# Optimization experiments

Measured on AMD Instinct MI355X. Metric: run time of the kernel, lower is better.

Reference implementation:

```python
import jax, jax.numpy as jnp
import numpy as np

D_MODEL = 1024
H = 16
HEAD_DIM = D_MODEL // H  # 64


def setup_inputs() -> dict:
    key = jax.random.key(0)
    ks = jax.random.split(key, 11)
    B, S, D = 1, 4096, D_MODEL
    scale = 1.0 / np.sqrt(D)
    inp = {
        'q': jax.random.normal(ks[0], (B, S, D), jnp.float32),
        'k': jax.random.normal(ks[1], (B, S, D), jnp.float32),
        'v': jax.random.normal(ks[2], (B, S, D), jnp.float32),
        'w_q': jax.random.normal(ks[3], (D, D), jnp.float32) * scale,
        'b_q': jnp.zeros((D,), jnp.float32),
        'w_k': jax.random.normal(ks[4], (D, D), jnp.float32) * scale,
        'b_k': jnp.zeros((D,), jnp.float32),
        'w_v': jax.random.normal(ks[5], (D, D), jnp.float32) * scale,
        'b_v': jnp.zeros((D,), jnp.float32),
        'w_o': jax.random.normal(ks[6], (D, D), jnp.float32) * scale,
        'b_o': jnp.zeros((D,), jnp.float32),
    }
    return inp


def reference(q, k, v, w_q, b_q, w_k, b_k, w_v, b_v, w_o, b_o):
    B, Sq, D = q.shape
    Sk = k.shape[1]
    # Linear projections (torch Linear: x @ W.T + b), split into heads: [B,H,S,hd]
    Q = (q @ w_q.T + b_q).reshape(B, Sq, H, HEAD_DIM).transpose(0, 2, 1, 3)
    K = (k @ w_k.T + b_k).reshape(B, Sk, H, HEAD_DIM).transpose(0, 2, 1, 3)
    V = (v @ w_v.T + b_v).reshape(B, Sk, H, HEAD_DIM).transpose(0, 2, 1, 3)
    # Naive attention: full [B,H,Sq,Sk] scores, softmax, then AV
    scores = jnp.einsum('bhqd,bhkd->bhqk', Q, K) / jnp.sqrt(jnp.float32(HEAD_DIM))
    attn = jax.nn.softmax(scores, axis=-1)
    ctx = jnp.einsum('bhqk,bhkd->bhqd', attn, V)
    concat = ctx.transpose(0, 2, 1, 3).reshape(B, Sq, D)
    return concat @ w_o.T + b_o
```

## Files before the change

### kernel.cpp

```cpp
#include <hip/hip_runtime.h>
#include <stdint.h>

#define S_LEN 4096
#define DM 1024
#define NH 16

typedef __attribute__((ext_vector_type(8))) short short8;
typedef __attribute__((ext_vector_type(4))) short short4v;
typedef __attribute__((ext_vector_type(4))) float float4v;
typedef __attribute__((ext_vector_type(4))) unsigned short ushort4v;

typedef __attribute__((address_space(1))) const void* as1cvp;
typedef __attribute__((address_space(3))) void* as3vp;

#define MFMA16(a, b, c) __builtin_amdgcn_mfma_f32_16x16x32_bf16((a), (b), (c), 0, 0, 0)
#define MFMA16K16(a, b, c) __builtin_amdgcn_mfma_f32_16x16x16bf16_1k((a), (b), (c), 0, 0, 0)
#define GLOAD_LDS16(g, l) \
  __builtin_amdgcn_global_load_lds((as1cvp)(g), (as3vp)(l), 16, 0, 0)

__device__ __forceinline__ unsigned short f2bf(float f) {
  unsigned u = __float_as_uint(f);
  u += 0x7fffu + ((u >> 16) & 1u);
  return (unsigned short)(u >> 16);
}

__device__ __forceinline__ float exp2_hw(float x) {
  float r;
  asm("v_exp_f32 %0, %1" : "=v"(r) : "v"(x));
  return r;
}

__global__ __launch_bounds__(256) void cast_all(
    const float* __restrict__ q, const float* __restrict__ k, const float* __restrict__ v,
    const float* __restrict__ wq, const float* __restrict__ wk, const float* __restrict__ wv,
    const float* __restrict__ wo, unsigned short* __restrict__ dst)
{
  const float* src; size_t off; int n;
  switch (blockIdx.y) {
    case 0: src = q;  off = 0u;        n = 4194304; break;
    case 1: src = k;  off = 4194304u;  n = 4194304; break;
    case 2: src = v;  off = 8388608u;  n = 4194304; break;
    case 3: src = wq; off = 12582912u; n = 1048576; break;
    case 4: src = wk; off = 13631488u; n = 1048576; break;
    case 5: src = wv; off = 14680064u; n = 1048576; break;
    default: src = wo; off = 15728640u; n = 1048576; break;
  }
  int nv = n >> 2;
  for (int i = blockIdx.x * blockDim.x + threadIdx.x; i < nv; i += gridDim.x * blockDim.x) {
    float4v val = ((const float4v*)src)[i];
    ushort4v o;
    o.x = f2bf(val.x); o.y = f2bf(val.y); o.z = f2bf(val.z); o.w = f2bf(val.w);
    ((ushort4v*)(dst + off))[i] = o;
  }
}

template<int MODE>
__device__ __forceinline__ void gemm128(
    const unsigned short* __restrict__ A, const unsigned short* __restrict__ Bw,
    unsigned short* Cb, float* Cf, const float* __restrict__ bias, float alpha,
    unsigned short* As, unsigned short* Bs)
{
  const int K = 1024, N = 1024;
  int bm = blockIdx.x, bn = blockIdx.y;
  int t = threadIdx.x, lane = t & 63, w = t >> 6;
  int l15 = lane & 15, l4 = lane >> 4;
  int wr = w >> 1, wc = w & 1;

  float4v acc[4][4] = {};

  for (int kt = 0; kt < K / 32; ++kt) {
#pragma unroll
    for (int i = 0; i < 2; ++i) {
      int ci = i * 256 + t;
      int r = ci >> 2, cb = ci & 3;
      GLOAD_LDS16(A + (size_t)(bm * 128 + r) * K + kt * 32 + cb * 8,
                  As + (size_t)(i * 256 + w * 64) * 8);
      GLOAD_LDS16(Bw + (size_t)(bn * 128 + r) * K + kt * 32 + cb * 8,
                  Bs + (size_t)(i * 256 + w * 64) * 8);
    }
    __syncthreads();
    short8 af[4], bfr[4];
#pragma unroll
    for (int mf = 0; mf < 4; ++mf)
      af[mf] = *(const short8*)&As[(wr * 64 + mf * 16 + l15) * 32 + l4 * 8];
#pragma unroll
    for (int nf = 0; nf < 4; ++nf)
      bfr[nf] = *(const short8*)&Bs[(wc * 64 + nf * 16 + l15) * 32 + l4 * 8];
#pragma unroll
    for (int mf = 0; mf < 4; ++mf)
#pragma unroll
      for (int nf = 0; nf < 4; ++nf)
        acc[mf][nf] = MFMA16(af[mf], bfr[nf], acc[mf][nf]);
    __syncthreads();
  }

#pragma unroll
  for (int mf = 0; mf < 4; ++mf)
#pragma unroll
    for (int nf = 0; nf < 4; ++nf) {
      int col = bn * 128 + wc * 64 + nf * 16 + l15;
      float bv = bias[col];
#pragma unroll
      for (int j = 0; j < 4; ++j) {
        int row = bm * 128 + wr * 64 + mf * 16 + l4 * 4 + j;
        float val = (acc[mf][nf][j] + bv) * alpha;
        if (MODE == 1)      Cf[(size_t)row * N + col] = val;
        else if (MODE == 2) Cb[(size_t)col * S_LEN + row] = f2bf(val);
        else                Cb[(size_t)row * N + col] = f2bf(val);
      }
    }
}

__global__ __launch_bounds__(256) void proj_qkv(
    const unsigned short* xq, const unsigned short* xk, const unsigned short* xv,
    const unsigned short* wq, const unsigned short* wk, const unsigned short* wv,
    unsigned short* Qp, unsigned short* Kp, unsigned short* Vt,
    const float* bq, const float* bk, const float* bv)
{
  __shared__ unsigned short As[128 * 32], Bs[128 * 32];
  switch (blockIdx.z) {
    case 0:  gemm128<0>(xq, wq, Qp, nullptr, bq, 0.1803368867f, As, Bs); break;
    case 1:  gemm128<0>(xk, wk, Kp, nullptr, bk, 1.0f,          As, Bs); break;
    default: gemm128<2>(xv, wv, Vt, nullptr, bv, 1.0f,          As, Bs); break;
  }
}

__global__ __launch_bounds__(256) void proj_o(
    const unsigned short* ctx, const unsigned short* wo, float* out, const float* bo)
{
  __shared__ unsigned short As[128 * 32], Bs[128 * 32];
  gemm128<1>(ctx, wo, nullptr, out, bo, 1.0f, As, Bs);
}

template<int BUF>
__device__ __forceinline__ void attn_tile(
    int kt,
    const unsigned short* kb0, const unsigned short* kb1,
    const int (&vAe)[4], const unsigned short* vbase,
    const unsigned short* kg, const unsigned short* vg,
    unsigned short* kls, unsigned short* vls,
    const short8 (&qf)[2], float4v (&acc_o)[4], float& m_run, float& l_run,
    int l4)
{
  if (kt + 1 < 64) {
    GLOAD_LDS16(kg + (size_t)(kt + 1) * (64 * DM), kls + (1 - BUF) * 4096);
    GLOAD_LDS16(vg + (kt + 1) * 64, vls + (1 - BUF) * 4096);
  }

  float4v sc[4];
#pragma unroll
  for (int nf = 0; nf < 4; ++nf) {
    short8 kf0 = *(const short8*)(kb0 + BUF * 4096 + nf * 1024);
    short8 kf1 = *(const short8*)(kb1 + BUF * 4096 + nf * 1024);
    float4v z = {0.f, 0.f, 0.f, 0.f};
    z = MFMA16(kf0, qf[0], z);
    sc[nf] = MFMA16(kf1, qf[1], z);
  }

  float mx = fmaxf(fmaxf(fmaxf(sc[0][0], sc[0][1]), sc[0][2]), sc[0][3]);
#pragma unroll
  for (int nf = 1; nf < 4; ++nf)
    mx = fmaxf(fmaxf(fmaxf(fmaxf(mx, sc[nf][0]), sc[nf][1]), sc[nf][2]), sc[nf][3]);
  mx = fmaxf(mx, __shfl_xor(mx, 16));
  mx = fmaxf(mx, __shfl_xor(mx, 32));

  if (!__all(mx <= m_run + 11.5f)) {
    float mnew = fmaxf(m_run, mx);
    float corr = exp2_hw(m_run - mnew);
    m_run = mnew;
    l_run *= corr;
#pragma unroll
    for (int j = 0; j < 4; ++j) {
      float cj = __shfl(corr, l4 * 4 + j);
#pragma unroll
      for (int nf2 = 0; nf2 < 4; ++nf2) acc_o[nf2][j] *= cj;
    }
  }

  float ps = 0.f;
  short4v pa[4];
#pragma unroll
  for (int nf = 0; nf < 4; ++nf) {
    float p0 = exp2_hw(sc[nf][0] - m_run);
    float p1 = exp2_hw(sc[nf][1] - m_run);
    float p2 = exp2_hw(sc[nf][2] - m_run);
    float p3 = exp2_hw(sc[nf][3] - m_run);
    ps += (p0 + p1) + (p2 + p3);
    unsigned lo, hi;
    asm("v_cvt_pk_bf16_f32 %0, %1, %2" : "=v"(lo) : "v"(p0), "v"(p1));
    asm("v_cvt_pk_bf16_f32 %0, %1, %2" : "=v"(hi) : "v"(p2), "v"(p3));
    union { unsigned u[2]; short4v s; } pk;
    pk.u[0] = lo; pk.u[1] = hi;
    pa[nf] = pk.s;
  }
  ps += __shfl_xor(ps, 16);
  ps += __shfl_xor(ps, 32);
  l_run += ps;

#pragma unroll
  for (int nfd = 0; nfd < 4; ++nfd)
#pragma unroll
    for (int nf = 0; nf < 4; ++nf) {
      short4v vf = *(const short4v*)(vbase + vAe[nf] + BUF * 4096 + nfd * 1024);
      acc_o[nfd] = MFMA16K16(pa[nf], vf, acc_o[nfd]);
    }

  __syncthreads();
}

__global__ __launch_bounds__(512) void attn_fused(
    const unsigned short* __restrict__ Qp, const unsigned short* __restrict__ Kp,
    const unsigned short* __restrict__ Vt, unsigned short* __restrict__ ctx)
{
  __shared__ unsigned short Ks[2][64 * 64];
  __shared__ unsigned short Vts[2][64 * 64];

  int bid = blockIdx.x;
  int wg = (bid & 7) * 64 + (bid >> 3);
  int h = wg >> 5, qt = wg & 31;

  int t = threadIdx.x, lane = t & 63, w = t >> 6;
  int l15 = lane & 15, l4 = lane >> 4;

  short8 qf[2];
  int qrow0 = qt * 128 + w * 16;
#pragma unroll
  for (int ks = 0; ks < 2; ++ks)
    qf[ks] = *(const short8*)&Qp[(size_t)(qrow0 + l15) * DM + h * 64 + ks * 32 + l4 * 8];

  float4v acc_o[4] = {};
  float m_run = -INFINITY, l_run = 0.f;

  const int swz = l15 & 7;
  const unsigned short* kb0 = &Ks[0][l15 * 64 + ((l4) ^ swz) * 8];
  const unsigned short* kb1 = &Ks[0][l15 * 64 + ((4 + l4) ^ swz) * 8];
  int vAe[4];
#pragma unroll
  for (int nf = 0; nf < 4; ++nf)
    vAe[nf] = l15 * 64 + (((2 * nf + (l4 >> 1)) ^ swz) * 8) + (l4 & 1) * 4;
  const unsigned short* vbase = &Vts[0][0];

  int sr = t >> 3, sp = t & 7;
  int slb = sp ^ (sr & 7);
  const unsigned short* kg = Kp + (size_t)sr * DM + h * 64 + slb * 8;
  const unsigned short* vg = Vt + (size_t)(h * 64 + sr) * S_LEN + slb * 8;
  unsigned short* kls = &Ks[0][t * 8];
  unsigned short* vls = &Vts[0][t * 8];

  GLOAD_LDS16(kg, kls);
  GLOAD_LDS16(vg, vls);
  __syncthreads();

  for (int kt = 0; kt < 64; kt += 2) {
    attn_tile<0>(kt,     kb0, kb1, vAe, vbase, kg, vg, kls, vls, qf, acc_o, m_run, l_run, l4);
    attn_tile<1>(kt + 1, kb0, kb1, vAe, vbase, kg, vg, kls, vls, qf, acc_o, m_run, l_run, l4);
  }

#pragma unroll
  for (int j = 0; j < 4; ++j) {
    float lj = __shfl(l_run, l4 * 4 + j);
    float inv = 1.0f / lj;
#pragma unroll
    for (int nfd = 0; nfd < 4; ++nfd) {
      int row = qrow0 + l4 * 4 + j;
      int col = h * 64 + nfd * 16 + l15;
      ctx[(size_t)row * DM + col] = f2bf(acc_o[nfd][j] * inv);
    }
  }
}

extern "C" void kernel_launch(void* const* d_in, const int* in_sizes, int n_in,
                              void* d_out, int out_size, void* d_ws, size_t ws_size,
                              hipStream_t stream) {
  const float* q  = (const float*)d_in[0];
  const float* k  = (const float*)d_in[1];
  const float* v  = (const float*)d_in[2];
  const float* wq = (const float*)d_in[3];
  const float* bq = (const float*)d_in[4];
  const float* wk = (const float*)d_in[5];
  const float* bk = (const float*)d_in[6];
  const float* wv = (const float*)d_in[7];
  const float* bv = (const float*)d_in[8];
  const float* wo = (const float*)d_in[9];
  const float* bo = (const float*)d_in[10];

  unsigned short* ws  = (unsigned short*)d_ws;
  unsigned short* qb  = ws;
  unsigned short* kb  = ws + 4194304u;
  unsigned short* vb  = ws + 8388608u;
  unsigned short* wqb = ws + 12582912u;
  unsigned short* wkb = ws + 13631488u;
  unsigned short* wvb = ws + 14680064u;
  unsigned short* wob = ws + 15728640u;
  unsigned short* Qp  = ws + 16777216u;
  unsigned short* Kp  = ws + 20971520u;
  unsigned short* Vt  = ws + 25165824u;
  unsigned short* ctx = qb;
  float* out = (float*)d_out;

  cast_all<<<dim3(1024, 7), 256, 0, stream>>>(q, k, v, wq, wk, wv, wo, ws);
  proj_qkv<<<dim3(32, 8, 3), 256, 0, stream>>>(qb, kb, vb, wqb, wkb, wvb, Qp, Kp, Vt, bq, bk, bv);
  attn_fused<<<dim3(512), 512, 0, stream>>>(Qp, Kp, Vt, ctx);
  proj_o<<<dim3(32, 8), 256, 0, stream>>>(ctx, wob, out, bo);
}
```

Baseline: 195.4 us.

## Split attention waves by query pairs and head-dim halves to reuse LDS fragments

Each pair of waves now shares 32 query rows instead of each wave owning 16. Each wave computes scores and softmax for both 16-row query fragments, but runs the PV product for only half of the 64 head dims. Each loaded K and V fragment is therefore reused across two query fragments, which cuts LDS read traffic per MFMA. The cost is that both waves in a pair repeat the QK^T MFMAs and the exp/softmax work. The per-tile cross-lane reduction of the row sum is also deferred to the epilogue.

```diff
diff --git a/kernel.cpp b/kernel.cpp
--- a/kernel.cpp
+++ b/kernel.cpp
@@ -139,70 +139,75 @@
     const int (&vAe)[4], const unsigned short* vbase,
     const unsigned short* kg, const unsigned short* vg,
     unsigned short* kls, unsigned short* vls,
-    const short8 (&qf)[2], float4v (&acc_o)[4], float& m_run, float& l_run,
-    int l4)
+    const short8 (&qf)[2][2], float4v (&acc_o)[2][2],
+    float (&m_run)[2], float (&l_run)[2], int l4)
 {
   if (kt + 1 < 64) {
     GLOAD_LDS16(kg + (size_t)(kt + 1) * (64 * DM), kls + (1 - BUF) * 4096);
     GLOAD_LDS16(vg + (kt + 1) * 64, vls + (1 - BUF) * 4096);
   }
 
-  float4v sc[4];
+  float4v sc[2][4];
 #pragma unroll
   for (int nf = 0; nf < 4; ++nf) {
     short8 kf0 = *(const short8*)(kb0 + BUF * 4096 + nf * 1024);
     short8 kf1 = *(const short8*)(kb1 + BUF * 4096 + nf * 1024);
-    float4v z = {0.f, 0.f, 0.f, 0.f};
-    z = MFMA16(kf0, qf[0], z);
-    sc[nf] = MFMA16(kf1, qf[1], z);
-  }
-
-  float mx = fmaxf(fmaxf(fmaxf(sc[0][0], sc[0][1]), sc[0][2]), sc[0][3]);
-#pragma unroll
-  for (int nf = 1; nf < 4; ++nf)
-    mx = fmaxf(fmaxf(fmaxf(fmaxf(mx, sc[nf][0]), sc[nf][1]), sc[nf][2]), sc[nf][3]);
-  mx = fmaxf(mx, __shfl_xor(mx, 16));
-  mx = fmaxf(mx, __shfl_xor(mx, 32));
-
-  if (!__all(mx <= m_run + 11.5f)) {
-    float mnew = fmaxf(m_run, mx);
-    float corr = exp2_hw(m_run - mnew);
-    m_run = mnew;
-    l_run *= corr;
-#pragma unroll
-    for (int j = 0; j < 4; ++j) {
-      float cj = __shfl(corr, l4 * 4 + j);
-#pragma unroll
-      for (int nf2 = 0; nf2 < 4; ++nf2) acc_o[nf2][j] *= cj;
-    }
-  }
-
-  float ps = 0.f;
-  short4v pa[4];
-#pragma unroll
-  for (int nf = 0; nf < 4; ++nf) {
-    float p0 = exp2_hw(sc[nf][0] - m_run);
-    float p1 = exp2_hw(sc[nf][1] - m_run);
-    float p2 = exp2_hw(sc[nf][2] - m_run);
-    float p3 = exp2_hw(sc[nf][3] - m_run);
-    ps += (p0 + p1) + (p2 + p3);
-    unsigned lo, hi;
-    asm("v_cvt_pk_bf16_f32 %0, %1, %2" : "=v"(lo) : "v"(p0), "v"(p1));
-    asm("v_cvt_pk_bf16_f32 %0, %1, %2" : "=v"(hi) : "v"(p2), "v"(p3));
-    union { unsigned u[2]; short4v s; } pk;
-    pk.u[0] = lo; pk.u[1] = hi;
-    pa[nf] = pk.s;
-  }
-  ps += __shfl_xor(ps, 16);
-  ps += __shfl_xor(ps, 32);
-  l_run += ps;
-
-#pragma unroll
-  for (int nfd = 0; nfd < 4; ++nfd)
+#pragma unroll
+    for (int mf = 0; mf < 2; ++mf) {
+      float4v z = {0.f, 0.f, 0.f, 0.f};
+      z = MFMA16(kf0, qf[mf][0], z);
+      sc[mf][nf] = MFMA16(kf1, qf[mf][1], z);
+    }
+  }
+
+  short4v pa[2][4];
+#pragma unroll
+  for (int mf = 0; mf < 2; ++mf) {
+    float mx = fmaxf(fmaxf(fmaxf(sc[mf][0][0], sc[mf][0][1]), sc[mf][0][2]), sc[mf][0][3]);
+#pragma unroll
+    for (int nf = 1; nf < 4; ++nf)
+      mx = fmaxf(fmaxf(fmaxf(fmaxf(mx, sc[mf][nf][0]), sc[mf][nf][1]), sc[mf][nf][2]), sc[mf][nf][3]);
+    mx = fmaxf(mx, __shfl_xor(mx, 16));
+    mx = fmaxf(mx, __shfl_xor(mx, 32));
+
+    if (!__all(mx <= m_run[mf] + 11.5f)) {
+      float mnew = fmaxf(m_run[mf], mx);
+      float corr = exp2_hw(m_run[mf] - mnew);
+      m_run[mf] = mnew;
+      l_run[mf] *= corr;
+#pragma unroll
+      for (int j = 0; j < 4; ++j) {
+        float cj = __shfl(corr, l4 * 4 + j);
+#pragma unroll
+        for (int i2 = 0; i2 < 2; ++i2) acc_o[mf][i2][j] *= cj;
+      }
+    }
+
+    float ps = 0.f;
 #pragma unroll
     for (int nf = 0; nf < 4; ++nf) {
-      short4v vf = *(const short4v*)(vbase + vAe[nf] + BUF * 4096 + nfd * 1024);
-      acc_o[nfd] = MFMA16K16(pa[nf], vf, acc_o[nfd]);
+      float p0 = exp2_hw(sc[mf][nf][0] - m_run[mf]);
+      float p1 = exp2_hw(sc[mf][nf][1] - m_run[mf]);
+      float p2 = exp2_hw(sc[mf][nf][2] - m_run[mf]);
+      float p3 = exp2_hw(sc[mf][nf][3] - m_run[mf]);
+      ps += (p0 + p1) + (p2 + p3);
+      unsigned lo, hi;
+      asm("v_cvt_pk_bf16_f32 %0, %1, %2" : "=v"(lo) : "v"(p0), "v"(p1));
+      asm("v_cvt_pk_bf16_f32 %0, %1, %2" : "=v"(hi) : "v"(p2), "v"(p3));
+      union { unsigned u[2]; short4v s; } pk;
+      pk.u[0] = lo; pk.u[1] = hi;
+      pa[mf][nf] = pk.s;
+    }
+    l_run[mf] += ps;
+  }
+
+#pragma unroll
+  for (int i = 0; i < 2; ++i)
+#pragma unroll
+    for (int nf = 0; nf < 4; ++nf) {
+      short4v vf = *(const short4v*)(vbase + vAe[nf] + BUF * 4096 + i * 1024);
+      acc_o[0][i] = MFMA16K16(pa[0][nf], vf, acc_o[0][i]);
+      acc_o[1][i] = MFMA16K16(pa[1][nf], vf, acc_o[1][i]);
     }
 
   __syncthreads();
@@ -221,15 +226,19 @@
 
   int t = threadIdx.x, lane = t & 63, w = t >> 6;
   int l15 = lane & 15, l4 = lane >> 4;
-
-  short8 qf[2];
-  int qrow0 = qt * 128 + w * 16;
-#pragma unroll
-  for (int ks = 0; ks < 2; ++ks)
-    qf[ks] = *(const short8*)&Qp[(size_t)(qrow0 + l15) * DM + h * 64 + ks * 32 + l4 * 8];
-
-  float4v acc_o[4] = {};
-  float m_run = -INFINITY, l_run = 0.f;
+  int qs = w >> 1, dh = w & 1;
+
+  short8 qf[2][2];
+  int qrow0 = qt * 128 + qs * 32;
+#pragma unroll
+  for (int mf = 0; mf < 2; ++mf)
+#pragma unroll
+    for (int ks = 0; ks < 2; ++ks)
+      qf[mf][ks] = *(const short8*)&Qp[(size_t)(qrow0 + mf * 16 + l15) * DM + h * 64 + ks * 32 + l4 * 8];
+
+  float4v acc_o[2][2] = {};
+  float m_run[2] = {-INFINITY, -INFINITY};
+  float l_run[2] = {0.f, 0.f};
 
   const int swz = l15 & 7;
   const unsigned short* kb0 = &Ks[0][l15 * 64 + ((l4) ^ swz) * 8];
@@ -238,7 +247,7 @@
 #pragma unroll
   for (int nf = 0; nf < 4; ++nf)
     vAe[nf] = l15 * 64 + (((2 * nf + (l4 >> 1)) ^ swz) * 8) + (l4 & 1) * 4;
-  const unsigned short* vbase = &Vts[0][0];
+  const unsigned short* vbase = &Vts[0][dh * 2048];
 
   int sr = t >> 3, sp = t & 7;
   int slb = sp ^ (sr & 7);
@@ -257,14 +266,20 @@
   }
 
 #pragma unroll
-  for (int j = 0; j < 4; ++j) {
-    float lj = __shfl(l_run, l4 * 4 + j);
-    float inv = 1.0f / lj;
-#pragma unroll
-    for (int nfd = 0; nfd < 4; ++nfd) {
-      int row = qrow0 + l4 * 4 + j;
-      int col = h * 64 + nfd * 16 + l15;
-      ctx[(size_t)row * DM + col] = f2bf(acc_o[nfd][j] * inv);
+  for (int mf = 0; mf < 2; ++mf) {
+    float lr = l_run[mf];
+    lr += __shfl_xor(lr, 16);
+    lr += __shfl_xor(lr, 32);
+#pragma unroll
+    for (int j = 0; j < 4; ++j) {
+      float lj = __shfl(lr, l4 * 4 + j);
+      float inv = 1.0f / lj;
+#pragma unroll
+      for (int i = 0; i < 2; ++i) {
+        int row = qrow0 + mf * 16 + l4 * 4 + j;
+        int col = h * 64 + dh * 32 + i * 16 + l15;
+        ctx[(size_t)row * DM + col] = f2bf(acc_o[mf][i][j] * inv);
+      }
     }
   }
 }
```

After: 231.1 us. 1.18x slower.

## Load V fragments directly from global and route P through per-wave LDS for K=32 MFMA

Applied to the files above, without the earlier changes.

Removes V staging in shared memory: each lane now reads its V fragments straight from global memory into registers, with no shared-memory copy. The probability tile is written to a per-wave padded LDS buffer and read back as 8-wide fragments, so the PV product uses 16x16x32 MFMAs in place of the 16x16x16 variant. The per-tile row-sum shuffles are deferred to the end of the loop. This trades the shared-memory V traffic and the extra MFMA count for uncached-latency global V loads, which every wave repeats, plus an LDS round-trip for P.

```diff
diff --git a/kernel.cpp b/kernel.cpp
--- a/kernel.cpp
+++ b/kernel.cpp
@@ -6,7 +6,6 @@
 #define NH 16
 
 typedef __attribute__((ext_vector_type(8))) short short8;
-typedef __attribute__((ext_vector_type(4))) short short4v;
 typedef __attribute__((ext_vector_type(4))) float float4v;
 typedef __attribute__((ext_vector_type(4))) unsigned short ushort4v;
 
@@ -14,7 +13,6 @@
 typedef __attribute__((address_space(3))) void* as3vp;
 
 #define MFMA16(a, b, c) __builtin_amdgcn_mfma_f32_16x16x32_bf16((a), (b), (c), 0, 0, 0)
-#define MFMA16K16(a, b, c) __builtin_amdgcn_mfma_f32_16x16x16bf16_1k((a), (b), (c), 0, 0, 0)
 #define GLOAD_LDS16(g, l) \
   __builtin_amdgcn_global_load_lds((as1cvp)(g), (as3vp)(l), 16, 0, 0)
 
@@ -136,16 +134,14 @@
 __device__ __forceinline__ void attn_tile(
     int kt,
     const unsigned short* kb0, const unsigned short* kb1,
-    const int (&vAe)[4], const unsigned short* vbase,
-    const unsigned short* kg, const unsigned short* vg,
-    unsigned short* kls, unsigned short* vls,
+    const unsigned short* const (&vrow)[4],
+    unsigned short* pw, const unsigned short* pr,
+    const unsigned short* kg, unsigned short* kls,
     const short8 (&qf)[2], float4v (&acc_o)[4], float& m_run, float& l_run,
     int l4)
 {
-  if (kt + 1 < 64) {
+  if (kt + 1 < 64)
     GLOAD_LDS16(kg + (size_t)(kt + 1) * (64 * DM), kls + (1 - BUF) * 4096);
-    GLOAD_LDS16(vg + (kt + 1) * 64, vls + (1 - BUF) * 4096);
-  }
 
   float4v sc[4];
 #pragma unroll
@@ -157,6 +153,14 @@
     sc[nf] = MFMA16(kf1, qf[1], z);
   }
 
+  short8 vf[4][2];
+  const int ktoff = kt * 64;
+#pragma unroll
+  for (int nfd = 0; nfd < 4; ++nfd)
+#pragma unroll
+    for (int kc = 0; kc < 2; ++kc)
+      vf[nfd][kc] = *(const short8*)(vrow[nfd] + ktoff + kc * 32);
+
   float mx = fmaxf(fmaxf(fmaxf(sc[0][0], sc[0][1]), sc[0][2]), sc[0][3]);
 #pragma unroll
   for (int nf = 1; nf < 4; ++nf)
@@ -178,7 +182,6 @@
   }
 
   float ps = 0.f;
-  short4v pa[4];
 #pragma unroll
   for (int nf = 0; nf < 4; ++nf) {
     float p0 = exp2_hw(sc[nf][0] - m_run);
@@ -189,22 +192,21 @@
     unsigned lo, hi;
     asm("v_cvt_pk_bf16_f32 %0, %1, %2" : "=v"(lo) : "v"(p0), "v"(p1));
     asm("v_cvt_pk_bf16_f32 %0, %1, %2" : "=v"(hi) : "v"(p2), "v"(p3));
-    union { unsigned u[2]; short4v s; } pk;
-    pk.u[0] = lo; pk.u[1] = hi;
-    pa[nf] = pk.s;
-  }
-  ps += __shfl_xor(ps, 16);
-  ps += __shfl_xor(ps, 32);
+    uint2 u; u.x = lo; u.y = hi;
+    *(uint2*)(pw + nf * 16) = u;
+  }
   l_run += ps;
 
-#pragma unroll
-  for (int nfd = 0; nfd < 4; ++nfd)
-#pragma unroll
-    for (int nf = 0; nf < 4; ++nf) {
-      short4v vf = *(const short4v*)(vbase + vAe[nf] + BUF * 4096 + nfd * 1024);
-      acc_o[nfd] = MFMA16K16(pa[nf], vf, acc_o[nfd]);
-    }
-
+  short8 pf[2];
+#pragma unroll
+  for (int kc = 0; kc < 2; ++kc)
+    pf[kc] = *(const short8*)(pr + kc * 32);
+
+#pragma unroll
+  for (int nfd = 0; nfd < 4; ++nfd) {
+    acc_o[nfd] = MFMA16(pf[0], vf[nfd][0], acc_o[nfd]);
+    acc_o[nfd] = MFMA16(pf[1], vf[nfd][1], acc_o[nfd]);
+  }
   __syncthreads();
 }
 
@@ -213,7 +215,7 @@
     const unsigned short* __restrict__ Vt, unsigned short* __restrict__ ctx)
 {
   __shared__ unsigned short Ks[2][64 * 64];
-  __shared__ unsigned short Vts[2][64 * 64];
+  __shared__ unsigned short Ps[8][16 * 72];
 
   int bid = blockIdx.x;
   int wg = (bid & 7) * 64 + (bid >> 3);
@@ -234,31 +236,33 @@
   const int swz = l15 & 7;
   const unsigned short* kb0 = &Ks[0][l15 * 64 + ((l4) ^ swz) * 8];
   const unsigned short* kb1 = &Ks[0][l15 * 64 + ((4 + l4) ^ swz) * 8];
-  int vAe[4];
-#pragma unroll
-  for (int nf = 0; nf < 4; ++nf)
-    vAe[nf] = l15 * 64 + (((2 * nf + (l4 >> 1)) ^ swz) * 8) + (l4 & 1) * 4;
-  const unsigned short* vbase = &Vts[0][0];
+  unsigned short* pw = &Ps[w][l15 * 72 + l4 * 4];
+  const unsigned short* pr = &Ps[w][l15 * 72 + l4 * 8];
+
+  const unsigned short* vrow[4];
+#pragma unroll
+  for (int nfd = 0; nfd < 4; ++nfd)
+    vrow[nfd] = Vt + (size_t)(h * 64 + nfd * 16 + l15) * S_LEN + l4 * 8;
 
   int sr = t >> 3, sp = t & 7;
   int slb = sp ^ (sr & 7);
   const unsigned short* kg = Kp + (size_t)sr * DM + h * 64 + slb * 8;
-  const unsigned short* vg = Vt + (size_t)(h * 64 + sr) * S_LEN + slb * 8;
   unsigned short* kls = &Ks[0][t * 8];
-  unsigned short* vls = &Vts[0][t * 8];
 
   GLOAD_LDS16(kg, kls);
-  GLOAD_LDS16(vg, vls);
   __syncthreads();
 
   for (int kt = 0; kt < 64; kt += 2) {
-    attn_tile<0>(kt,     kb0, kb1, vAe, vbase, kg, vg, kls, vls, qf, acc_o, m_run, l_run, l4);
-    attn_tile<1>(kt + 1, kb0, kb1, vAe, vbase, kg, vg, kls, vls, qf, acc_o, m_run, l_run, l4);
-  }
-
+    attn_tile<0>(kt,     kb0, kb1, vrow, pw, pr, kg, kls, qf, acc_o, m_run, l_run, l4);
+    attn_tile<1>(kt + 1, kb0, kb1, vrow, pw, pr, kg, kls, qf, acc_o, m_run, l_run, l4);
+  }
+
+  float lr = l_run;
+  lr += __shfl_xor(lr, 16);
+  lr += __shfl_xor(lr, 32);
 #pragma unroll
   for (int j = 0; j < 4; ++j) {
-    float lj = __shfl(l_run, l4 * 4 + j);
+    float lj = __shfl(lr, l4 * 4 + j);
     float inv = 1.0f / lj;
 #pragma unroll
     for (int nfd = 0; nfd < 4; ++nfd) {
```

Measured after the change: 330.2 us. 1.69x slower.
